# Optimization experiments

Hardware: AMD Instinct MI355X
Metric: run time of the kernel (lower is better)

Reference implementation:

```python
import jax, jax.numpy as jnp
import numpy as np

N_VOCAB = 100000
N_FIELDS = 40
K = 64
ATTN = 64
BATCH = 2048

def setup_inputs() -> dict:
    key = jax.random.key(0)
    ks = jax.random.split(key, 9)
    x = jax.random.randint(ks[0], (BATCH, N_FIELDS), 0, N_VOCAB)
    lin_table = jax.random.normal(ks[1], (N_VOCAB, 1), dtype=jnp.float32) * 0.01
    V_table = jax.random.normal(ks[2], (N_VOCAB, K), dtype=jnp.float32) * 0.01
    W1 = jax.random.normal(ks[3], (K, ATTN), dtype=jnp.float32) * (1.0 / np.sqrt(K))
    b1 = jnp.zeros((ATTN,), dtype=jnp.float32)
    W2 = jax.random.normal(ks[4], (ATTN, 1), dtype=jnp.float32) * (1.0 / np.sqrt(ATTN))
    b2 = jnp.zeros((1,), dtype=jnp.float32)
    Wf = jax.random.normal(ks[5], (K, 1), dtype=jnp.float32) * (1.0 / np.sqrt(K))
    bf = jnp.zeros((1,), dtype=jnp.float32)
    return {"x": x, "lin_table": lin_table, "V_table": V_table,
            "W1": W1, "b1": b1, "W2": W2, "b2": b2, "Wf": Wf, "bf": bf}

def reference(x, lin_table, V_table, W1, b1, W2, b2, Wf, bf):
    # linear part: sum of per-feature scalar weights -> [B, 1]
    linear_part = jnp.sum(lin_table[x], axis=1)
    # embeddings: [B, F, K]
    embd = V_table[x]
    # pairwise interactions: [B, F, F, K]
    pw = embd[:, :, None, :] * embd[:, None, :, :]
    # attention MLP: k -> attn -> 1, scores [B, F, F, 1]
    h = jax.nn.relu(jnp.einsum('bijk,ka->bija', pw, W1) + b1)
    scores = jnp.einsum('bija,ao->bijo', h, W2) + b2
    # softmax over dim=2 (second field axis)
    probs = jax.nn.softmax(scores, axis=2)
    # weighted sum over j then i -> [B, K]
    weighted = jnp.sum(probs * pw, axis=2)
    weighted_embd = jnp.sum(weighted, axis=1)
    interaction_part = weighted_embd @ Wf + bf  # [B, 1]
    return jax.nn.sigmoid(linear_part + interaction_part)[:, 0]
```

## Files before the change

kernel.cpp:

```cpp
#include <hip/hip_runtime.h>

#define NF 40
#define KD 64

typedef float f32x4 __attribute__((ext_vector_type(4)));
typedef _Float16 f16x8 __attribute__((ext_vector_type(8)));
typedef _Float16 f16x4 __attribute__((ext_vector_type(4)));

__global__ __launch_bounds__(256, 4)
void afm_kernel(const int* __restrict__ x,
                const float* __restrict__ lin_table,
                const float* __restrict__ V_table,
                const float* __restrict__ W1,
                const float* __restrict__ b1,
                const float* __restrict__ W2,
                const float* __restrict__ b2,
                const float* __restrict__ Wf,
                const float* __restrict__ bf,
                float* __restrict__ out)
{
    __shared__ _Float16 e16[64][72];
    __shared__ _Float16 Q16[48][72];
    __shared__ unsigned short lut[832];
    __shared__ float zbuf[48];
    __shared__ float webuf[4][KD];
    __shared__ float linbuf[64];

    const int b = blockIdx.x;
    const int tid = threadIdx.x;
    const int w = tid >> 6;
    const int lane = tid & 63;
    const int l15 = lane & 15;
    const int lhi = lane >> 4;

    {
        f16x8 zh = {0, 0, 0, 0, 0, 0, 0, 0};
        for (int t = tid; t < 48 * 72 / 8; t += 256)
            reinterpret_cast<f16x8*>(&Q16[0][0])[t] = zh;
        if (tid < 216)
            reinterpret_cast<f16x8*>(&e16[40][0])[tid] = zh;
        if (tid < 48) zbuf[tid] = 1.0f;
        reinterpret_cast<float*>(webuf)[tid] = 0.0f;
    }
    for (int p0 = tid; p0 < 832; p0 += 256) {
        int p = p0 > 819 ? 819 : p0;
        int i = (int)((81.0f - sqrtf(6561.0f - 8.0f * (float)p)) * 0.5f);
        int off = (i * (81 - i)) >> 1;
        if ((((i + 1) * (80 - i)) >> 1) <= p) { ++i; off = (i * (81 - i)) >> 1; }
        else if (off > p)                   { --i; off = (i * (81 - i)) >> 1; }
        int j = i + (p - off);
        lut[p0] = (unsigned short)((i << 8) | j);
    }

    f16x8 Af[4][2];
    #pragma unroll
    for (int at = 0; at < 4; ++at) {
        #pragma unroll
        for (int ks = 0; ks < 2; ++ks) {
            f16x8 t;
            #pragma unroll
            for (int el = 0; el < 8; ++el)
                t[el] = (_Float16)W1[(ks * 32 + lhi * 8 + el) * KD + at * 16 + l15];
            Af[at][ks] = t;
        }
    }
    f32x4 b1v[4], w2v[4];
    #pragma unroll
    for (int at = 0; at < 4; ++at) {
        #pragma unroll
        for (int r = 0; r < 4; ++r) {
            b1v[at][r] = b1[at * 16 + lhi * 4 + r];
            w2v[at][r] = W2[at * 16 + lhi * 4 + r];
        }
    }
    const float Wfv = Wf[lane];

    for (int q = tid; q < NF * (KD / 4); q += 256) {
        int i = q >> 4;
        int k4 = q & 15;
        int ix = x[b * NF + i];
        float4 v = reinterpret_cast<const float4*>(V_table + (size_t)ix * KD)[k4];
        f16x4 hv = {(_Float16)v.x, (_Float16)v.y, (_Float16)v.z, (_Float16)v.w};
        *reinterpret_cast<f16x4*>(&e16[i][k4 * 4]) = hv;
    }
    if (tid < 64) linbuf[tid] = (tid < NF) ? lin_table[x[b * NF + tid]] : 0.0f;
    __syncthreads();

    for (int mt = w; mt < 52; mt += 4) {
        const int v = lut[mt * 16 + l15];
        const int i = v >> 8;
        const int j = v & 255;

        const _Float16* ei = &e16[i][0];
        const _Float16* ej = &e16[j][0];
        const int k0 = lhi * 8;
        f16x8 B0 = (*reinterpret_cast<const f16x8*>(ei + k0)) *
                   (*reinterpret_cast<const f16x8*>(ej + k0));
        f16x8 B1 = (*reinterpret_cast<const f16x8*>(ei + k0 + 32)) *
                   (*reinterpret_cast<const f16x8*>(ej + k0 + 32));

        f32x4 d[4];
        #pragma unroll
        for (int at = 0; at < 4; ++at) {
            d[at] = b1v[at];
            d[at] = __builtin_amdgcn_mfma_f32_16x16x32_f16(Af[at][0], B0, d[at], 0, 0, 0);
            d[at] = __builtin_amdgcn_mfma_f32_16x16x32_f16(Af[at][1], B1, d[at], 0, 0, 0);
        }

        float s = 0.0f;
        #pragma unroll
        for (int at = 0; at < 4; ++at) {
            #pragma unroll
            for (int r = 0; r < 4; ++r)
                s = fmaf(fmaxf(d[at][r], 0.0f), w2v[at][r], s);
        }
        s += __shfl_xor(s, 16, 64);
        s += __shfl_xor(s, 32, 64);
        float qv = __expf(s);
        if (lhi == 0) {
            _Float16 qh = (_Float16)qv;
            Q16[i][j] = qh;
            Q16[j][i] = qh;
        }
    }
    __syncthreads();

    f32x4 gd[4];
    #pragma unroll
    for (int it = 0; it < 4; ++it) gd[it] = (f32x4){0.f, 0.f, 0.f, 0.f};

    #pragma unroll
    for (int it = 0; it < 4; ++it) {
        const int t = w + it * 4;
        if (t < 15) {
            const int mt = (t * 52) >> 8;
            const int nt = t - mt * 5;

            const _Float16* qrow = &Q16[mt * 16 + l15][0];
            f16x8 aq0 = *reinterpret_cast<const f16x8*>(qrow + lhi * 8);
            f16x8 aq1 = *reinterpret_cast<const f16x8*>(qrow + 32 + lhi * 8);

            f16x8 bv0, bv1;
            if (nt == 4) {
                _Float16 one1 = (l15 == 0) ? (_Float16)1.0f : (_Float16)0.0f;
                #pragma unroll
                for (int el = 0; el < 8; ++el) {
                    bv0[el] = one1;
                    bv1[el] = (lhi == 0) ? one1 : (_Float16)0.0f;
                }
            } else {
                const int c = nt * 16 + l15;
                #pragma unroll
                for (int el = 0; el < 8; ++el) {
                    bv0[el] = e16[lhi * 8 + el][c];
                    bv1[el] = e16[32 + lhi * 8 + el][c];
                }
            }

            f32x4 dq = {0.f, 0.f, 0.f, 0.f};
            dq = __builtin_amdgcn_mfma_f32_16x16x32_f16(aq0, bv0, dq, 0, 0, 0);
            dq = __builtin_amdgcn_mfma_f32_16x16x32_f16(aq1, bv1, dq, 0, 0, 0);

            if (nt == 4) {
                #pragma unroll
                for (int r = 0; r < 4; ++r) {
                    int ii = mt * 16 + lhi * 4 + r;
                    if (l15 == 0 && ii < 40) zbuf[ii] = dq[r];
                }
            } else {
                gd[it] = dq;
            }
        }
    }
    __syncthreads();

    #pragma unroll
    for (int it = 0; it < 4; ++it) {
        const int t = w + it * 4;
        if (t < 15) {
            const int mt = (t * 52) >> 8;
            const int nt = t - mt * 5;
            if (nt != 4) {
                const int c = nt * 16 + l15;
                float acc = 0.0f;
                #pragma unroll
                for (int r = 0; r < 4; ++r) {
                    int ii = mt * 16 + lhi * 4 + r;
                    float ev = (float)e16[ii][c];
                    acc = fmaf(ev * gd[it][r],
                               __builtin_amdgcn_rcpf(zbuf[ii]), acc);
                }
                acc += __shfl_xor(acc, 16, 64);
                acc += __shfl_xor(acc, 32, 64);
                if (lhi == 0) webuf[w][c] = acc;
            }
        }
    }
    __syncthreads();

    if (w == 0) {
        float we = webuf[0][lane] + webuf[1][lane] + webuf[2][lane] + webuf[3][lane];
        float c = fmaf(we, Wfv, linbuf[lane]);
        #pragma unroll
        for (int off = 32; off > 0; off >>= 1)
            c += __shfl_xor(c, off, 64);
        if (lane == 0) {
            float z = c + bf[0];
            out[b] = 1.0f / (1.0f + __expf(-z));
        }
    }
}

extern "C" void kernel_launch(void* const* d_in, const int* in_sizes, int n_in,
                              void* d_out, int out_size, void* d_ws, size_t ws_size,
                              hipStream_t stream) {
    const int*   x         = (const int*)d_in[0];
    const float* lin_table = (const float*)d_in[1];
    const float* V_table   = (const float*)d_in[2];
    const float* W1        = (const float*)d_in[3];
    const float* b1        = (const float*)d_in[4];
    const float* W2        = (const float*)d_in[5];
    const float* b2        = (const float*)d_in[6];
    const float* Wf        = (const float*)d_in[7];
    const float* bf        = (const float*)d_in[8];
    float* out = (float*)d_out;

    const int batch = in_sizes[0] / NF;
    afm_kernel<<<batch, 256, 0, stream>>>(x, lin_table, V_table, W1, b1, W2, b2,
                                          Wf, bf, out);
}
```

Baseline: 35.22 us.

## Assign one sample per wavefront instead of one per block

Each 256-thread block now processes four samples, one per wave, with per-wave LDS buffers. The block-wide barriers between the pair-scoring, aggregation and reduction stages become wave-local barriers. Softmax normalisation and the final reductions stay in registers and shuffles instead of going through shared buffers. This removes cross-wave synchronisation and LDS round trips, but each wave now runs all 52 pair tiles serially, and LDS per block roughly quadruples, which may lower occupancy.

```diff
diff --git a/kernel.cpp b/kernel.cpp
--- a/kernel.cpp
+++ b/kernel.cpp
@@ -19,38 +19,50 @@
                 const float* __restrict__ bf,
                 float* __restrict__ out)
 {
-    __shared__ _Float16 e16[64][72];
-    __shared__ _Float16 Q16[48][72];
+    __shared__ _Float16 ew[4][NF][72];
+    __shared__ _Float16 Qw[4][48][72];
     __shared__ unsigned short lut[832];
-    __shared__ float zbuf[48];
-    __shared__ float webuf[4][KD];
-    __shared__ float linbuf[64];
-
-    const int b = blockIdx.x;
+
     const int tid = threadIdx.x;
     const int w = tid >> 6;
     const int lane = tid & 63;
     const int l15 = lane & 15;
     const int lhi = lane >> 4;
-
-    {
-        f16x8 zh = {0, 0, 0, 0, 0, 0, 0, 0};
-        for (int t = tid; t < 48 * 72 / 8; t += 256)
-            reinterpret_cast<f16x8*>(&Q16[0][0])[t] = zh;
-        if (tid < 216)
-            reinterpret_cast<f16x8*>(&e16[40][0])[tid] = zh;
-        if (tid < 48) zbuf[tid] = 1.0f;
-        reinterpret_cast<float*>(webuf)[tid] = 0.0f;
-    }
+    const int smp = blockIdx.x * 4 + w;
+
     for (int p0 = tid; p0 < 832; p0 += 256) {
         int p = p0 > 819 ? 819 : p0;
         int i = (int)((81.0f - sqrtf(6561.0f - 8.0f * (float)p)) * 0.5f);
         int off = (i * (81 - i)) >> 1;
         if ((((i + 1) * (80 - i)) >> 1) <= p) { ++i; off = (i * (81 - i)) >> 1; }
-        else if (off > p)                   { --i; off = (i * (81 - i)) >> 1; }
-        int j = i + (p - off);
-        lut[p0] = (unsigned short)((i << 8) | j);
-    }
+        else if (off > p)                     { --i; off = (i * (81 - i)) >> 1; }
+        lut[p0] = (unsigned short)((i << 8) | (i + (p - off)));
+    }
+
+    _Float16* e = &ew[w][0][0];
+    _Float16* Q = &Qw[w][0][0];
+
+    {
+        f16x8 zh = {0, 0, 0, 0, 0, 0, 0, 0};
+        for (int t = lane; t < 192; t += 64) {
+            if (t < 120) {
+                int r = t / 3, c8 = t - r * 3;
+                *reinterpret_cast<f16x8*>(Q + r * 72 + 40 + c8 * 8) = zh;
+            } else {
+                int t2 = t - 120, r9 = t2 / 9;
+                *reinterpret_cast<f16x8*>(Q + (40 + r9) * 72 + (t2 - r9 * 9) * 8) = zh;
+            }
+        }
+    }
+
+    for (int q = lane; q < NF * (KD / 4); q += 64) {
+        int i = q >> 4, k4 = q & 15;
+        int ix = x[smp * NF + i];
+        float4 v = reinterpret_cast<const float4*>(V_table + (size_t)ix * KD)[k4];
+        f16x4 hv = {(_Float16)v.x, (_Float16)v.y, (_Float16)v.z, (_Float16)v.w};
+        *reinterpret_cast<f16x4*>(e + i * 72 + k4 * 4) = hv;
+    }
+    float linv = (lane < NF) ? lin_table[x[smp * NF + lane]] : 0.0f;
 
     f16x8 Af[4][2];
     #pragma unroll
@@ -67,33 +79,24 @@
     f32x4 b1v[4], w2v[4];
     #pragma unroll
     for (int at = 0; at < 4; ++at) {
-        #pragma unroll
-        for (int r = 0; r < 4; ++r) {
-            b1v[at][r] = b1[at * 16 + lhi * 4 + r];
-            w2v[at][r] = W2[at * 16 + lhi * 4 + r];
-        }
-    }
-    const float Wfv = Wf[lane];
-
-    for (int q = tid; q < NF * (KD / 4); q += 256) {
-        int i = q >> 4;
-        int k4 = q & 15;
-        int ix = x[b * NF + i];
-        float4 v = reinterpret_cast<const float4*>(V_table + (size_t)ix * KD)[k4];
-        f16x4 hv = {(_Float16)v.x, (_Float16)v.y, (_Float16)v.z, (_Float16)v.w};
-        *reinterpret_cast<f16x4*>(&e16[i][k4 * 4]) = hv;
-    }
-    if (tid < 64) linbuf[tid] = (tid < NF) ? lin_table[x[b * NF + tid]] : 0.0f;
+        b1v[at] = *reinterpret_cast<const f32x4*>(b1 + at * 16 + lhi * 4);
+        w2v[at] = *reinterpret_cast<const f32x4*>(W2 + at * 16 + lhi * 4);
+    }
+    float wfv[4];
+    #pragma unroll
+    for (int nt = 0; nt < 4; ++nt) wfv[nt] = Wf[nt * 16 + l15];
+    const float bf0 = bf[0];
+
     __syncthreads();
-
-    for (int mt = w; mt < 52; mt += 4) {
+    __builtin_amdgcn_wave_barrier();
+
+    const int k0 = lhi * 8;
+    for (int mt = 0; mt < 52; ++mt) {
         const int v = lut[mt * 16 + l15];
         const int i = v >> 8;
         const int j = v & 255;
-
-        const _Float16* ei = &e16[i][0];
-        const _Float16* ej = &e16[j][0];
-        const int k0 = lhi * 8;
+        const _Float16* ei = e + i * 72;
+        const _Float16* ej = e + j * 72;
         f16x8 B0 = (*reinterpret_cast<const f16x8*>(ei + k0)) *
                    (*reinterpret_cast<const f16x8*>(ej + k0));
         f16x8 B1 = (*reinterpret_cast<const f16x8*>(ei + k0 + 32)) *
@@ -119,95 +122,83 @@
         float qv = __expf(s);
         if (lhi == 0) {
             _Float16 qh = (_Float16)qv;
-            Q16[i][j] = qh;
-            Q16[j][i] = qh;
-        }
-    }
-    __syncthreads();
-
-    f32x4 gd[4];
-    #pragma unroll
-    for (int it = 0; it < 4; ++it) gd[it] = (f32x4){0.f, 0.f, 0.f, 0.f};
-
-    #pragma unroll
-    for (int it = 0; it < 4; ++it) {
-        const int t = w + it * 4;
-        if (t < 15) {
-            const int mt = (t * 52) >> 8;
-            const int nt = t - mt * 5;
-
-            const _Float16* qrow = &Q16[mt * 16 + l15][0];
-            f16x8 aq0 = *reinterpret_cast<const f16x8*>(qrow + lhi * 8);
-            f16x8 aq1 = *reinterpret_cast<const f16x8*>(qrow + 32 + lhi * 8);
-
+            Q[i * 72 + j] = qh;
+            Q[j * 72 + i] = qh;
+        }
+    }
+    __builtin_amdgcn_wave_barrier();
+
+    float acc4[4] = {0.f, 0.f, 0.f, 0.f};
+    #pragma unroll
+    for (int mt = 0; mt < 3; ++mt) {
+        const _Float16* qrow = Q + (mt * 16 + l15) * 72;
+        f16x8 aq0 = *reinterpret_cast<const f16x8*>(qrow + lhi * 8);
+        f16x8 aq1 = *reinterpret_cast<const f16x8*>(qrow + 32 + lhi * 8);
+
+        f16x8 one0, one1;
+        #pragma unroll
+        for (int el = 0; el < 8; ++el) {
+            one0[el] = (_Float16)1.0f;
+            one1[el] = (lhi == 0) ? (_Float16)1.0f : (_Float16)0.0f;
+        }
+        f32x4 dz = {0.f, 0.f, 0.f, 0.f};
+        dz = __builtin_amdgcn_mfma_f32_16x16x32_f16(aq0, one0, dz, 0, 0, 0);
+        dz = __builtin_amdgcn_mfma_f32_16x16x32_f16(aq1, one1, dz, 0, 0, 0);
+        float rz[4];
+        #pragma unroll
+        for (int r = 0; r < 4; ++r) {
+            int ii = mt * 16 + lhi * 4 + r;
+            rz[r] = (ii < NF) ? __builtin_amdgcn_rcpf(dz[r]) : 0.0f;
+        }
+
+        #pragma unroll
+        for (int nt = 0; nt < 4; ++nt) {
+            const int c = nt * 16 + l15;
             f16x8 bv0, bv1;
-            if (nt == 4) {
-                _Float16 one1 = (l15 == 0) ? (_Float16)1.0f : (_Float16)0.0f;
-                #pragma unroll
-                for (int el = 0; el < 8; ++el) {
-                    bv0[el] = one1;
-                    bv1[el] = (lhi == 0) ? one1 : (_Float16)0.0f;
-                }
-            } else {
-                const int c = nt * 16 + l15;
-                #pragma unroll
-                for (int el = 0; el < 8; ++el) {
-                    bv0[el] = e16[lhi * 8 + el][c];
-                    bv1[el] = e16[32 + lhi * 8 + el][c];
-                }
+            #pragma unroll
+            for (int el = 0; el < 8; ++el) {
+                bv0[el] = e[(lhi * 8 + el) * 72 + c];
+                bv1[el] = (lhi == 0) ? e[(32 + el) * 72 + c]
+                                     : (_Float16)0.0f;
             }
-
             f32x4 dq = {0.f, 0.f, 0.f, 0.f};
             dq = __builtin_amdgcn_mfma_f32_16x16x32_f16(aq0, bv0, dq, 0, 0, 0);
             dq = __builtin_amdgcn_mfma_f32_16x16x32_f16(aq1, bv1, dq, 0, 0, 0);
 
-            if (nt == 4) {
-                #pragma unroll
-                for (int r = 0; r < 4; ++r) {
-                    int ii = mt * 16 + lhi * 4 + r;
-                    if (l15 == 0 && ii < 40) zbuf[ii] = dq[r];
-                }
-            } else {
-                gd[it] = dq;
+            float a = 0.0f;
+            #pragma unroll
+            for (int r = 0; r < 4; ++r) {
+                int ii = mt * 16 + lhi * 4 + r;
+                int iic = ii > 39 ? 39 : ii;
+                a = fmaf((float)e[iic * 72 + c] * dq[r], rz[r], a);
             }
-        }
-    }
-    __syncthreads();
-
-    #pragma unroll
-    for (int it = 0; it < 4; ++it) {
-        const int t = w + it * 4;
-        if (t < 15) {
-            const int mt = (t * 52) >> 8;
-            const int nt = t - mt * 5;
-            if (nt != 4) {
-                const int c = nt * 16 + l15;
-                float acc = 0.0f;
-                #pragma unroll
-                for (int r = 0; r < 4; ++r) {
-                    int ii = mt * 16 + lhi * 4 + r;
-                    float ev = (float)e16[ii][c];
-                    acc = fmaf(ev * gd[it][r],
-                               __builtin_amdgcn_rcpf(zbuf[ii]), acc);
-                }
-                acc += __shfl_xor(acc, 16, 64);
-                acc += __shfl_xor(acc, 32, 64);
-                if (lhi == 0) webuf[w][c] = acc;
-            }
-        }
-    }
-    __syncthreads();
-
-    if (w == 0) {
-        float we = webuf[0][lane] + webuf[1][lane] + webuf[2][lane] + webuf[3][lane];
-        float c = fmaf(we, Wfv, linbuf[lane]);
-        #pragma unroll
-        for (int off = 32; off > 0; off >>= 1)
-            c += __shfl_xor(c, off, 64);
-        if (lane == 0) {
-            float z = c + bf[0];
-            out[b] = 1.0f / (1.0f + __expf(-z));
-        }
+            acc4[nt] += a;
+        }
+    }
+
+    #pragma unroll
+    for (int nt = 0; nt < 4; ++nt) {
+        acc4[nt] += __shfl_xor(acc4[nt], 16, 64);
+        acc4[nt] += __shfl_xor(acc4[nt], 32, 64);
+    }
+    float inter = 0.0f;
+    #pragma unroll
+    for (int nt = 0; nt < 4; ++nt) inter = fmaf(acc4[nt], wfv[nt], inter);
+    inter += __shfl_xor(inter, 1, 64);
+    inter += __shfl_xor(inter, 2, 64);
+    inter += __shfl_xor(inter, 4, 64);
+    inter += __shfl_xor(inter, 8, 64);
+
+    linv += __shfl_xor(linv, 32, 64);
+    linv += __shfl_xor(linv, 16, 64);
+    linv += __shfl_xor(linv, 8, 64);
+    linv += __shfl_xor(linv, 4, 64);
+    linv += __shfl_xor(linv, 2, 64);
+    linv += __shfl_xor(linv, 1, 64);
+
+    if (lane == 0) {
+        float z = linv + inter + bf0;
+        out[smp] = 1.0f / (1.0f + __expf(-z));
     }
 }
 
@@ -226,6 +217,6 @@
     float* out = (float*)d_out;
 
     const int batch = in_sizes[0] / NF;
-    afm_kernel<<<batch, 256, 0, stream>>>(x, lin_table, V_table, W1, b1, W2, b2,
-                                          Wf, bf, out);
+    afm_kernel<<<batch / 4, 256, 0, stream>>>(x, lin_table, V_table, W1, b1, W2,
+                                              b2, Wf, bf, out);
 }
```

New measurement: 40.28 us. +14.3%, slower.
